# Kernel optimization log

Hardware: AMD Instinct MI355X
Metric: run time of the kernel (lower is better)

## Reference

```python
import jax, jax.numpy as jnp
import numpy as np

EMB = 1024
N_HEAD = 16
D_QK = 128  # emb_dim // h_qk
D_V = 128   # emb_dim // h_v


def setup_inputs() -> dict:
    key = jax.random.key(0)
    ks = jax.random.split(key, 9)
    s_in = 1.0 / np.sqrt(EMB)
    s_pr = 1.0 / np.sqrt(N_HEAD * D_V)
    return {
        "X": jax.random.normal(ks[0], (2, 2048, EMB), dtype=jnp.float32),
        "Wq": jax.random.uniform(ks[1], (EMB, N_HEAD * D_QK), jnp.float32, -s_in, s_in),
        "bq": jax.random.uniform(ks[2], (N_HEAD * D_QK,), jnp.float32, -s_in, s_in),
        "Wk": jax.random.uniform(ks[3], (EMB, N_HEAD * D_QK), jnp.float32, -s_in, s_in),
        "bk": jax.random.uniform(ks[4], (N_HEAD * D_QK,), jnp.float32, -s_in, s_in),
        "Wv": jax.random.uniform(ks[5], (EMB, N_HEAD * D_V), jnp.float32, -s_in, s_in),
        "bv": jax.random.uniform(ks[6], (N_HEAD * D_V,), jnp.float32, -s_in, s_in),
        "Wp": jax.random.uniform(ks[7], (N_HEAD * D_V, EMB), jnp.float32, -s_pr, s_pr),
        "bp": jax.random.uniform(ks[8], (EMB,), jnp.float32, -s_pr, s_pr),
    }


def reference(X, Wq, bq, Wk, bk, Wv, bv, Wp, bp):
    b, t, d = X.shape
    # projections -> (b, h, t, dh)
    Q = (X @ Wq + bq).reshape(b, t, N_HEAD, D_QK).transpose(0, 2, 1, 3)
    K = (X @ Wk + bk).reshape(b, t, N_HEAD, D_QK).transpose(0, 2, 1, 3)
    V = (X @ Wv + bv).reshape(b, t, N_HEAD, D_V).transpose(0, 2, 1, 3)
    scale = 1.0 / jnp.sqrt(jnp.asarray(D_QK, X.dtype))
    att = jnp.einsum("bhqd,bhkd->bhqk", Q, K) * scale  # (b,h,t,t)
    causal = jnp.tril(jnp.ones((t, t), dtype=bool))
    att = jnp.where(causal[None, None], att, jnp.asarray(-jnp.inf, att.dtype))
    att = jax.nn.softmax(att, axis=-1)
    y = jnp.einsum("bhqk,bhkd->bhqd", att, V)
    y = y.transpose(0, 2, 1, 3).reshape(b, t, N_HEAD * D_V)
    return y @ Wp + bp
```

## Files before the change

### kernel.cpp

```cpp
#include <hip/hip_runtime.h>
#include <hip/hip_bf16.h>
#include <math.h>

#define EMB   1024
#define NHEAD 16
#define DHEAD 128
#define TSEQ  2048
#define NB    2
#define MROWS (NB * TSEQ)
#define QKVN  (NHEAD * DHEAD)

typedef __bf16 bf16x8 __attribute__((ext_vector_type(8)));
typedef __bf16 bf16x4 __attribute__((ext_vector_type(4)));
typedef float  f32x4  __attribute__((ext_vector_type(4)));

__global__ __launch_bounds__(256) void cast_to_bf16(
    const float* __restrict__ in, __bf16* __restrict__ out) {
  int i = (blockIdx.x * 256 + threadIdx.x) * 4;
  float4 v = *(const float4*)(in + i);
  bf16x4 o = {(__bf16)v.x, (__bf16)v.y, (__bf16)v.z, (__bf16)v.w};
  *(bf16x4*)(out + i) = o;
}

__global__ __launch_bounds__(256) void cast_transpose(
    const float* __restrict__ in, __bf16* __restrict__ out, int K, int N) {
  __shared__ __bf16 tile[32][33];
  const int k0 = blockIdx.y * 32;
  const int n0 = blockIdx.x * 32;
  const int c = threadIdx.x & 31;
  const int r = threadIdx.x >> 5;
#pragma unroll
  for (int i = 0; i < 4; ++i) {
    int kk = r + i * 8;
    tile[kk][c] = (__bf16)in[(size_t)(k0 + kk) * N + n0 + c];
  }
  __syncthreads();
#pragma unroll
  for (int i = 0; i < 4; ++i) {
    int nn = r + i * 8;
    out[(size_t)(n0 + nn) * K + k0 + c] = tile[c][nn];
  }
}

__global__ __launch_bounds__(256) void transpose_v(
    const __bf16* __restrict__ Vb, __bf16* __restrict__ Vt) {
  __shared__ __bf16 tile[32][34];
  const int bh = blockIdx.z;
  const int b = bh >> 4, h = bh & 15;
  const int t0 = blockIdx.y * 32;
  const int d0 = blockIdx.x * 32;
  const int c = threadIdx.x & 31;
  const int r = threadIdx.x >> 5;
#pragma unroll
  for (int i = 0; i < 4; ++i) {
    int tt = r + i * 8;
    tile[tt][c] = Vb[(size_t)(b * TSEQ + t0 + tt) * QKVN + h * DHEAD + d0 + c];
  }
  __syncthreads();
#pragma unroll
  for (int i = 0; i < 4; ++i) {
    int dd = r + i * 8;
    Vt[((size_t)bh * DHEAD + d0 + dd) * TSEQ + t0 + c] = tile[c][dd];
  }
}

__device__ __forceinline__ void store1(float* p, float v) { *p = v; }
__device__ __forceinline__ void store1(__bf16* p, float v) { *p = (__bf16)v; }

template <typename OT>
__device__ __forceinline__ void gemm_core(
    const __bf16* __restrict__ A, const __bf16* __restrict__ Bt,
    const float* __restrict__ bias, OT* __restrict__ C,
    int N, int K, int brow, int bcol, float osc,
    __bf16* As, __bf16* Bs) {
  const int tid = threadIdx.x;
  const int wv = tid >> 6, ln = tid & 63;
  const int wr = wv >> 1, wc = wv & 1;
  const int cl = ln & 15, gp = ln >> 4;

  f32x4 acc[4][4];
#pragma unroll
  for (int i = 0; i < 4; ++i)
#pragma unroll
    for (int j = 0; j < 4; ++j) acc[i][j] = (f32x4){0.f, 0.f, 0.f, 0.f};

  for (int k0 = 0; k0 < K; k0 += 64) {
#pragma unroll
    for (int i = 0; i < 4; ++i) {
      int idx = i * 256 + tid;
      int r = idx >> 3, cp = idx & 7;
      int c = cp ^ (r & 7);
      const __bf16* ga = A + (size_t)(brow + r) * K + k0 + c * 8;
      __builtin_amdgcn_global_load_lds(
          (const __attribute__((address_space(1))) unsigned int*)ga,
          (__attribute__((address_space(3))) unsigned int*)(As + (size_t)(i * 256 + wv * 64) * 8),
          16, 0, 0);
      const __bf16* gb = Bt + (size_t)(bcol + r) * K + k0 + c * 8;
      __builtin_amdgcn_global_load_lds(
          (const __attribute__((address_space(1))) unsigned int*)gb,
          (__attribute__((address_space(3))) unsigned int*)(Bs + (size_t)(i * 256 + wv * 64) * 8),
          16, 0, 0);
    }
    __syncthreads();

#pragma unroll
    for (int kc = 0; kc < 2; ++kc) {
      bf16x8 af[4], bfr[4];
#pragma unroll
      for (int i = 0; i < 4; ++i) {
        int r = wr * 64 + i * 16 + cl;
        int c = kc * 4 + gp;
        af[i] = *(const bf16x8*)(As + ((size_t)(r * 8 + (c ^ (r & 7)))) * 8);
      }
#pragma unroll
      for (int j = 0; j < 4; ++j) {
        int r = wc * 64 + j * 16 + cl;
        int c = kc * 4 + gp;
        bfr[j] = *(const bf16x8*)(Bs + ((size_t)(r * 8 + (c ^ (r & 7)))) * 8);
      }
#pragma unroll
      for (int i = 0; i < 4; ++i)
#pragma unroll
        for (int j = 0; j < 4; ++j)
          acc[i][j] = __builtin_amdgcn_mfma_f32_16x16x32_bf16(af[i], bfr[j], acc[i][j], 0, 0, 0);
    }
    __syncthreads();
  }

#pragma unroll
  for (int j = 0; j < 4; ++j) {
    int col = bcol + wc * 64 + j * 16 + cl;
    float bb = bias[col];
#pragma unroll
    for (int i = 0; i < 4; ++i) {
#pragma unroll
      for (int rr = 0; rr < 4; ++rr) {
        int row = brow + wr * 64 + i * 16 + gp * 4 + rr;
        store1(C + (size_t)row * N + col, (acc[i][j][rr] + bb) * osc);
      }
    }
  }
}

__global__ __launch_bounds__(256) void gemm_qkv(
    const __bf16* __restrict__ A,
    const __bf16* __restrict__ Wqt, const __bf16* __restrict__ Wkt, const __bf16* __restrict__ Wvt,
    const float* __restrict__ bq, const float* __restrict__ bk, const float* __restrict__ bv,
    __bf16* __restrict__ Q, __bf16* __restrict__ Ko, __bf16* __restrict__ V) {
  __shared__ __bf16 As[8192], Bs[8192];
  const int z = blockIdx.z;
  const __bf16* Bt = z == 0 ? Wqt : z == 1 ? Wkt : Wvt;
  const float* bias = z == 0 ? bq : z == 1 ? bk : bv;
  __bf16* C = z == 0 ? Q : z == 1 ? Ko : V;
  float osc = z == 0 ? 0.08838834764831845f : 1.0f;
  gemm_core<__bf16>(A, Bt, bias, C, QKVN, EMB, blockIdx.y * 128, blockIdx.x * 128, osc, As, Bs);
}

__global__ __launch_bounds__(256) void gemm_proj(
    const __bf16* __restrict__ A, const __bf16* __restrict__ Bt,
    const float* __restrict__ bias, float* __restrict__ C) {
  __shared__ __bf16 As[8192], Bs[8192];
  gemm_core<float>(A, Bt, bias, C, EMB, QKVN, blockIdx.y * 128, blockIdx.x * 128, 1.0f, As, Bs);
}

__device__ __forceinline__ void attn_stage(
    const __bf16* __restrict__ Kg, const __bf16* __restrict__ Vg,
    __bf16* Kbuf, __bf16* Vbuf, int kt, int wv, int ln) {
#pragma unroll
  for (int i = 0; i < 4; ++i) {
    int seg = wv * 4 + i;
    int u = seg * 4 + (ln >> 4);
    int slot = ln & 15;
    int xk = slot ^ (u & 15);
    const __bf16* gk = Kg + (size_t)(kt * 64 + u) * QKVN + xk * 8;
    __builtin_amdgcn_global_load_lds(
        (const __attribute__((address_space(1))) unsigned int*)gk,
        (__attribute__((address_space(3))) unsigned int*)(Kbuf + seg * 512), 16, 0, 0);
    int d = 2 * u + (xk & 1);
    int c2 = xk >> 1;
    const __bf16* gv = Vg + (size_t)d * TSEQ + kt * 64 + c2 * 8;
    __builtin_amdgcn_global_load_lds(
        (const __attribute__((address_space(1))) unsigned int*)gv,
        (__attribute__((address_space(3))) unsigned int*)(Vbuf + seg * 512), 16, 0, 0);
  }
}

__global__ __launch_bounds__(256, 2) void attn_mfma(
    const __bf16* __restrict__ Qb, const __bf16* __restrict__ Kb,
    const __bf16* __restrict__ Vt, __bf16* __restrict__ Y) {
  __shared__ __bf16 Ks[2][8192];
  __shared__ __bf16 Vs[2][8192];
  __shared__ __bf16 Ps[4][2048];

  const int tid = threadIdx.x;
  const int wv = tid >> 6, ln = tid & 63;
  const int cl = ln & 15, gp = ln >> 4;

  const int x = blockIdx.x;
  const int bh = x & 31;
  const int qt = 15 - (x >> 5);
  const int b = bh >> 4, h = bh & 15;
  const int ntiles = 2 * qt + 2;
  const int qloc = qt * 128 + wv * 32;
  const size_t grow = (size_t)b * TSEQ + qloc;

  bf16x8 qa[2][4];
#pragma unroll
  for (int i = 0; i < 2; ++i)
#pragma unroll
    for (int kc = 0; kc < 4; ++kc)
      qa[i][kc] = *(const bf16x8*)(Qb + (grow + i * 16 + cl) * QKVN + h * DHEAD + kc * 32 + gp * 8);

  f32x4 o[2][8];
  f32x4 lacc[2];
#pragma unroll
  for (int i = 0; i < 2; ++i) {
    lacc[i] = (f32x4){0.f, 0.f, 0.f, 0.f};
#pragma unroll
    for (int n = 0; n < 8; ++n) o[i][n] = (f32x4){0.f, 0.f, 0.f, 0.f};
  }
  const __bf16 one_b = (__bf16)1.0f;
  const bf16x8 ones = {one_b, one_b, one_b, one_b, one_b, one_b, one_b, one_b};

  const __bf16* Kg = Kb + (size_t)b * TSEQ * QKVN + h * DHEAD;
  const __bf16* Vg = Vt + (size_t)bh * DHEAD * TSEQ;

  attn_stage(Kg, Vg, Ks[0], Vs[0], 0, wv, ln);
  __syncthreads();

  for (int kt = 0; kt < ntiles; ++kt) {
    const int cur = kt & 1;
    if (kt + 1 < ntiles)
      attn_stage(Kg, Vg, Ks[cur ^ 1], Vs[cur ^ 1], kt + 1, wv, ln);

    if (kt * 64 <= qloc + 31) {
      f32x4 sacc[2][4];
#pragma unroll
      for (int i = 0; i < 2; ++i)
#pragma unroll
        for (int s = 0; s < 4; ++s) sacc[i][s] = (f32x4){0.f, 0.f, 0.f, 0.f};
#pragma unroll
      for (int kc = 0; kc < 4; ++kc) {
#pragma unroll
        for (int s = 0; s < 4; ++s) {
          int r = s * 16 + cl;
          bf16x8 kfr = *(const bf16x8*)(&Ks[cur][r * 128 + (((kc * 4 + gp) ^ (r & 15)) * 8)]);
          sacc[0][s] = __builtin_amdgcn_mfma_f32_16x16x32_bf16(qa[0][kc], kfr, sacc[0][s], 0, 0, 0);
          sacc[1][s] = __builtin_amdgcn_mfma_f32_16x16x32_bf16(qa[1][kc], kfr, sacc[1][s], 0, 0, 0);
        }
      }
      const bool diag = (kt * 64 + 63 > qloc);
#pragma unroll
      for (int i = 0; i < 2; ++i)
#pragma unroll
        for (int s = 0; s < 4; ++s) {
          int key = kt * 64 + s * 16 + cl;
#pragma unroll
          for (int rg = 0; rg < 4; ++rg) {
            int q = i * 16 + gp * 4 + rg;
            float pv = __expf(sacc[i][s][rg]);
            if (diag && key > qloc + q) pv = 0.f;
            Ps[wv][(s * 2 + (cl >> 3)) * 256 + q * 8 + (cl & 7)] = (__bf16)pv;
          }
        }
      bf16x8 pfr[2][2];
#pragma unroll
      for (int i = 0; i < 2; ++i)
#pragma unroll
        for (int k2 = 0; k2 < 2; ++k2)
          pfr[i][k2] = *(const bf16x8*)(&Ps[wv][(k2 * 4 + gp) * 256 + (i * 16 + cl) * 8]);
#pragma unroll
      for (int i = 0; i < 2; ++i)
#pragma unroll
        for (int k2 = 0; k2 < 2; ++k2)
          lacc[i] = __builtin_amdgcn_mfma_f32_16x16x32_bf16(pfr[i][k2], ones, lacc[i], 0, 0, 0);
#pragma unroll
      for (int n = 0; n < 8; ++n) {
#pragma unroll
        for (int k2 = 0; k2 < 2; ++k2) {
          int d = n * 16 + cl;
          int u = d >> 1;
          int xv = ((k2 * 4 + gp) << 1) | (d & 1);
          bf16x8 vfr = *(const bf16x8*)(&Vs[cur][u * 128 + ((xv ^ (u & 15)) * 8)]);
          o[0][n] = __builtin_amdgcn_mfma_f32_16x16x32_bf16(pfr[0][k2], vfr, o[0][n], 0, 0, 0);
          o[1][n] = __builtin_amdgcn_mfma_f32_16x16x32_bf16(pfr[1][k2], vfr, o[1][n], 0, 0, 0);
        }
      }
    }
    __syncthreads();
  }

#pragma unroll
  for (int i = 0; i < 2; ++i) {
    f32x4 inv;
#pragma unroll
    for (int rg = 0; rg < 4; ++rg) inv[rg] = 1.0f / lacc[i][rg];
#pragma unroll
    for (int n = 0; n < 8; ++n)
#pragma unroll
      for (int rg = 0; rg < 4; ++rg) {
        __bf16* yp = Y + (grow + i * 16 + gp * 4 + rg) * QKVN + h * DHEAD + n * 16 + cl;
        *yp = (__bf16)(o[i][n][rg] * inv[rg]);
      }
  }
}

extern "C" void kernel_launch(void* const* d_in, const int* in_sizes, int n_in,
                              void* d_out, int out_size, void* d_ws, size_t ws_size,
                              hipStream_t stream) {
  const float* X  = (const float*)d_in[0];
  const float* Wq = (const float*)d_in[1];
  const float* bq = (const float*)d_in[2];
  const float* Wk = (const float*)d_in[3];
  const float* bk = (const float*)d_in[4];
  const float* Wv = (const float*)d_in[5];
  const float* bv = (const float*)d_in[6];
  const float* Wp = (const float*)d_in[7];
  const float* bp = (const float*)d_in[8];
  float* out = (float*)d_out;

  const size_t xsz = (size_t)MROWS * EMB;
  const size_t wsz = (size_t)EMB * QKVN;
  const size_t msz = (size_t)MROWS * QKVN;
  __bf16* Xb  = (__bf16*)d_ws;
  __bf16* Wqt = Xb + xsz;
  __bf16* Wkt = Wqt + wsz;
  __bf16* Wvt = Wkt + wsz;
  __bf16* Wpt = Wvt + wsz;
  __bf16* Qb  = Wpt + wsz;
  __bf16* Kb  = Qb + msz;
  __bf16* Vb  = Kb + msz;
  __bf16* Vtb = Vb + msz;
  __bf16* Yb  = Vtb + msz;

  dim3 blk(256);

  cast_to_bf16<<<dim3(xsz / 1024), blk, 0, stream>>>(X, Xb);
  cast_transpose<<<dim3(QKVN / 32, EMB / 32), blk, 0, stream>>>(Wq, Wqt, EMB, QKVN);
  cast_transpose<<<dim3(QKVN / 32, EMB / 32), blk, 0, stream>>>(Wk, Wkt, EMB, QKVN);
  cast_transpose<<<dim3(QKVN / 32, EMB / 32), blk, 0, stream>>>(Wv, Wvt, EMB, QKVN);
  cast_transpose<<<dim3(EMB / 32, QKVN / 32), blk, 0, stream>>>(Wp, Wpt, QKVN, EMB);

  gemm_qkv<<<dim3(QKVN / 128, MROWS / 128, 3), blk, 0, stream>>>(
      Xb, Wqt, Wkt, Wvt, bq, bk, bv, Qb, Kb, Vb);

  transpose_v<<<dim3(DHEAD / 32, TSEQ / 32, NB * NHEAD), blk, 0, stream>>>(Vb, Vtb);

  attn_mfma<<<dim3(512), blk, 0, stream>>>(Qb, Kb, Vtb, Yb);

  gemm_proj<<<dim3(EMB / 128, MROWS / 128), blk, 0, stream>>>(Yb, Wpt, bp, out);
}
```

Before: 312.7 us.

## Fuse prep kernels, write V transposed from GEMM, keep P in registers, retile projection

Merges the X cast and the four weight cast-transposes into one prep launch. The QKV GEMM epilogue now writes V directly in head-transposed layout, so the separate transpose_v kernel and its buffer go away. Attention swaps MFMA operand order so P stays in registers: it is built with cross-lane shuffles instead of an LDS round trip, and row sums come from shuffle reductions instead of a ones-matrix MFMA. Output stores are vectorized, and the projection GEMM uses 64-row tiles to double the block count. Several independent changes increase the risk of layout or indexing mistakes.

```diff
diff --git a/kernel.cpp b/kernel.cpp
--- a/kernel.cpp
+++ b/kernel.cpp
@@ -14,60 +14,55 @@
 typedef __bf16 bf16x4 __attribute__((ext_vector_type(4)));
 typedef float  f32x4  __attribute__((ext_vector_type(4)));
 
-__global__ __launch_bounds__(256) void cast_to_bf16(
-    const float* __restrict__ in, __bf16* __restrict__ out) {
-  int i = (blockIdx.x * 256 + threadIdx.x) * 4;
-  float4 v = *(const float4*)(in + i);
-  bf16x4 o = {(__bf16)v.x, (__bf16)v.y, (__bf16)v.z, (__bf16)v.w};
-  *(bf16x4*)(out + i) = o;
-}
-
-__global__ __launch_bounds__(256) void cast_transpose(
-    const float* __restrict__ in, __bf16* __restrict__ out, int K, int N) {
+__device__ __forceinline__ unsigned pk_bf16(float a, float b) {
+  union { __bf16 h; unsigned short u; } ca, cb;
+  ca.h = (__bf16)a; cb.h = (__bf16)b;
+  return (unsigned)ca.u | ((unsigned)cb.u << 16);
+}
+
+__global__ __launch_bounds__(256) void prep(
+    const float* __restrict__ X,
+    const float* __restrict__ Wq, const float* __restrict__ Wk,
+    const float* __restrict__ Wv, const float* __restrict__ Wp,
+    __bf16* __restrict__ Xb, __bf16* __restrict__ Wqt, __bf16* __restrict__ Wkt,
+    __bf16* __restrict__ Wvt, __bf16* __restrict__ Wpt) {
+  const int z = blockIdx.z;
+  if (z == 4) {
+    size_t id = ((size_t)(blockIdx.y * 64 + blockIdx.x)) * 2048 + threadIdx.x * 8;
+    float4 v0 = *(const float4*)(X + id);
+    float4 v1 = *(const float4*)(X + id + 4);
+    bf16x8 o = {(__bf16)v0.x, (__bf16)v0.y, (__bf16)v0.z, (__bf16)v0.w,
+                (__bf16)v1.x, (__bf16)v1.y, (__bf16)v1.z, (__bf16)v1.w};
+    *(bf16x8*)(Xb + id) = o;
+    return;
+  }
   __shared__ __bf16 tile[32][33];
-  const int k0 = blockIdx.y * 32;
-  const int n0 = blockIdx.x * 32;
-  const int c = threadIdx.x & 31;
-  const int r = threadIdx.x >> 5;
+  const float* in; __bf16* out; int K_, N_, k0, n0;
+  if (z < 3) {
+    in = z == 0 ? Wq : z == 1 ? Wk : Wv;
+    out = z == 0 ? Wqt : z == 1 ? Wkt : Wvt;
+    K_ = EMB; N_ = QKVN; k0 = blockIdx.y * 32; n0 = blockIdx.x * 32;
+  } else {
+    in = Wp; out = Wpt; K_ = QKVN; N_ = EMB; k0 = blockIdx.x * 32; n0 = blockIdx.y * 32;
+  }
+  const int c = threadIdx.x & 31, r = threadIdx.x >> 5;
 #pragma unroll
   for (int i = 0; i < 4; ++i) {
     int kk = r + i * 8;
-    tile[kk][c] = (__bf16)in[(size_t)(k0 + kk) * N + n0 + c];
+    tile[kk][c] = (__bf16)in[(size_t)(k0 + kk) * N_ + n0 + c];
   }
   __syncthreads();
 #pragma unroll
   for (int i = 0; i < 4; ++i) {
     int nn = r + i * 8;
-    out[(size_t)(n0 + nn) * K + k0 + c] = tile[c][nn];
-  }
-}
-
-__global__ __launch_bounds__(256) void transpose_v(
-    const __bf16* __restrict__ Vb, __bf16* __restrict__ Vt) {
-  __shared__ __bf16 tile[32][34];
-  const int bh = blockIdx.z;
-  const int b = bh >> 4, h = bh & 15;
-  const int t0 = blockIdx.y * 32;
-  const int d0 = blockIdx.x * 32;
-  const int c = threadIdx.x & 31;
-  const int r = threadIdx.x >> 5;
-#pragma unroll
-  for (int i = 0; i < 4; ++i) {
-    int tt = r + i * 8;
-    tile[tt][c] = Vb[(size_t)(b * TSEQ + t0 + tt) * QKVN + h * DHEAD + d0 + c];
-  }
-  __syncthreads();
-#pragma unroll
-  for (int i = 0; i < 4; ++i) {
-    int dd = r + i * 8;
-    Vt[((size_t)bh * DHEAD + d0 + dd) * TSEQ + t0 + c] = tile[c][dd];
+    out[(size_t)(n0 + nn) * K_ + k0 + c] = tile[c][nn];
   }
 }
 
 __device__ __forceinline__ void store1(float* p, float v) { *p = v; }
 __device__ __forceinline__ void store1(__bf16* p, float v) { *p = (__bf16)v; }
 
-template <typename OT>
+template <int TM, typename OT, bool VT>
 __device__ __forceinline__ void gemm_core(
     const __bf16* __restrict__ A, const __bf16* __restrict__ Bt,
     const float* __restrict__ bias, OT* __restrict__ C,
@@ -75,29 +70,33 @@
     __bf16* As, __bf16* Bs) {
   const int tid = threadIdx.x;
   const int wv = tid >> 6, ln = tid & 63;
-  const int wr = wv >> 1, wc = wv & 1;
   const int cl = ln & 15, gp = ln >> 4;
-
-  f32x4 acc[4][4];
+  constexpr int SJ = (TM == 128) ? 4 : 2;
+  const int rbase = (TM == 128) ? (wv >> 1) * 64 : 0;
+  const int cbase = (TM == 128) ? (wv & 1) * 64 : wv * 32;
+
+  f32x4 acc[4][SJ];
 #pragma unroll
   for (int i = 0; i < 4; ++i)
 #pragma unroll
-    for (int j = 0; j < 4; ++j) acc[i][j] = (f32x4){0.f, 0.f, 0.f, 0.f};
+    for (int j = 0; j < SJ; ++j) acc[i][j] = (f32x4){0.f, 0.f, 0.f, 0.f};
 
   for (int k0 = 0; k0 < K; k0 += 64) {
+#pragma unroll
+    for (int i = 0; i < TM / 32; ++i) {
+      int idx = i * 256 + tid;
+      int r = idx >> 3, cp = idx & 7, c = cp ^ (r & 7);
+      __builtin_amdgcn_global_load_lds(
+          (const __attribute__((address_space(1))) unsigned int*)(A + (size_t)(brow + r) * K + k0 + c * 8),
+          (__attribute__((address_space(3))) unsigned int*)(As + (size_t)(i * 256 + wv * 64) * 8),
+          16, 0, 0);
+    }
 #pragma unroll
     for (int i = 0; i < 4; ++i) {
       int idx = i * 256 + tid;
-      int r = idx >> 3, cp = idx & 7;
-      int c = cp ^ (r & 7);
-      const __bf16* ga = A + (size_t)(brow + r) * K + k0 + c * 8;
+      int r = idx >> 3, cp = idx & 7, c = cp ^ (r & 7);
       __builtin_amdgcn_global_load_lds(
-          (const __attribute__((address_space(1))) unsigned int*)ga,
-          (__attribute__((address_space(3))) unsigned int*)(As + (size_t)(i * 256 + wv * 64) * 8),
-          16, 0, 0);
-      const __bf16* gb = Bt + (size_t)(bcol + r) * K + k0 + c * 8;
-      __builtin_amdgcn_global_load_lds(
-          (const __attribute__((address_space(1))) unsigned int*)gb,
+          (const __attribute__((address_space(1))) unsigned int*)(Bt + (size_t)(bcol + r) * K + k0 + c * 8),
           (__attribute__((address_space(3))) unsigned int*)(Bs + (size_t)(i * 256 + wv * 64) * 8),
           16, 0, 0);
     }
@@ -105,38 +104,56 @@
 
 #pragma unroll
     for (int kc = 0; kc < 2; ++kc) {
-      bf16x8 af[4], bfr[4];
+      bf16x8 af[4], bfr[SJ];
 #pragma unroll
       for (int i = 0; i < 4; ++i) {
-        int r = wr * 64 + i * 16 + cl;
+        int r = rbase + i * 16 + cl;
         int c = kc * 4 + gp;
         af[i] = *(const bf16x8*)(As + ((size_t)(r * 8 + (c ^ (r & 7)))) * 8);
       }
 #pragma unroll
-      for (int j = 0; j < 4; ++j) {
-        int r = wc * 64 + j * 16 + cl;
+      for (int j = 0; j < SJ; ++j) {
+        int r = cbase + j * 16 + cl;
         int c = kc * 4 + gp;
         bfr[j] = *(const bf16x8*)(Bs + ((size_t)(r * 8 + (c ^ (r & 7)))) * 8);
       }
 #pragma unroll
       for (int i = 0; i < 4; ++i)
 #pragma unroll
-        for (int j = 0; j < 4; ++j)
+        for (int j = 0; j < SJ; ++j)
           acc[i][j] = __builtin_amdgcn_mfma_f32_16x16x32_bf16(af[i], bfr[j], acc[i][j], 0, 0, 0);
     }
     __syncthreads();
   }
 
-#pragma unroll
-  for (int j = 0; j < 4; ++j) {
-    int col = bcol + wc * 64 + j * 16 + cl;
-    float bb = bias[col];
-#pragma unroll
-    for (int i = 0; i < 4; ++i) {
-#pragma unroll
-      for (int rr = 0; rr < 4; ++rr) {
-        int row = brow + wr * 64 + i * 16 + gp * 4 + rr;
-        store1(C + (size_t)row * N + col, (acc[i][j][rr] + bb) * osc);
+  if constexpr (VT) {
+#pragma unroll
+    for (int j = 0; j < SJ; ++j) {
+      int col = bcol + cbase + j * 16 + cl;
+      float bb = bias[col];
+      int hh = col >> 7, dh = col & 127;
+#pragma unroll
+      for (int i = 0; i < 4; ++i) {
+        int row = brow + rbase + i * 16 + gp * 4;
+        int bi = row >> 11, t = row & 2047;
+        __bf16* p = (__bf16*)C + ((size_t)((bi * NHEAD + hh) * DHEAD + dh)) * TSEQ + t;
+        bf16x4 st = {(__bf16)((acc[i][j][0] + bb) * osc), (__bf16)((acc[i][j][1] + bb) * osc),
+                     (__bf16)((acc[i][j][2] + bb) * osc), (__bf16)((acc[i][j][3] + bb) * osc)};
+        *(bf16x4*)p = st;
+      }
+    }
+  } else {
+#pragma unroll
+    for (int j = 0; j < SJ; ++j) {
+      int col = bcol + cbase + j * 16 + cl;
+      float bb = bias[col];
+#pragma unroll
+      for (int i = 0; i < 4; ++i) {
+#pragma unroll
+        for (int rr = 0; rr < 4; ++rr) {
+          int row = brow + rbase + i * 16 + gp * 4 + rr;
+          store1(C + (size_t)row * N + col, (acc[i][j][rr] + bb) * osc);
+        }
       }
     }
   }
@@ -146,21 +163,27 @@
     const __bf16* __restrict__ A,
     const __bf16* __restrict__ Wqt, const __bf16* __restrict__ Wkt, const __bf16* __restrict__ Wvt,
     const float* __restrict__ bq, const float* __restrict__ bk, const float* __restrict__ bv,
-    __bf16* __restrict__ Q, __bf16* __restrict__ Ko, __bf16* __restrict__ V) {
+    __bf16* __restrict__ Q, __bf16* __restrict__ Ko, __bf16* __restrict__ Vt) {
   __shared__ __bf16 As[8192], Bs[8192];
   const int z = blockIdx.z;
-  const __bf16* Bt = z == 0 ? Wqt : z == 1 ? Wkt : Wvt;
-  const float* bias = z == 0 ? bq : z == 1 ? bk : bv;
-  __bf16* C = z == 0 ? Q : z == 1 ? Ko : V;
-  float osc = z == 0 ? 0.08838834764831845f : 1.0f;
-  gemm_core<__bf16>(A, Bt, bias, C, QKVN, EMB, blockIdx.y * 128, blockIdx.x * 128, osc, As, Bs);
+  if (z == 0) {
+    gemm_core<128, __bf16, false>(A, Wqt, bq, Q, QKVN, EMB, blockIdx.y * 128, blockIdx.x * 128,
+                                  0.08838834764831845f, As, Bs);
+  } else if (z == 1) {
+    gemm_core<128, __bf16, false>(A, Wkt, bk, Ko, QKVN, EMB, blockIdx.y * 128, blockIdx.x * 128,
+                                  1.0f, As, Bs);
+  } else {
+    gemm_core<128, __bf16, true>(A, Wvt, bv, Vt, QKVN, EMB, blockIdx.y * 128, blockIdx.x * 128,
+                                 1.0f, As, Bs);
+  }
 }
 
 __global__ __launch_bounds__(256) void gemm_proj(
     const __bf16* __restrict__ A, const __bf16* __restrict__ Bt,
     const float* __restrict__ bias, float* __restrict__ C) {
-  __shared__ __bf16 As[8192], Bs[8192];
-  gemm_core<float>(A, Bt, bias, C, EMB, QKVN, blockIdx.y * 128, blockIdx.x * 128, 1.0f, As, Bs);
+  __shared__ __bf16 As[4096], Bs[8192];
+  gemm_core<64, float, false>(A, Bt, bias, C, EMB, QKVN, blockIdx.y * 64, blockIdx.x * 128,
+                              1.0f, As, Bs);
 }
 
 __device__ __forceinline__ void attn_stage(
@@ -172,15 +195,12 @@
     int u = seg * 4 + (ln >> 4);
     int slot = ln & 15;
     int xk = slot ^ (u & 15);
-    const __bf16* gk = Kg + (size_t)(kt * 64 + u) * QKVN + xk * 8;
     __builtin_amdgcn_global_load_lds(
-        (const __attribute__((address_space(1))) unsigned int*)gk,
+        (const __attribute__((address_space(1))) unsigned int*)(Kg + (size_t)(kt * 64 + u) * QKVN + xk * 8),
         (__attribute__((address_space(3))) unsigned int*)(Kbuf + seg * 512), 16, 0, 0);
-    int d = 2 * u + (xk & 1);
-    int c2 = xk >> 1;
-    const __bf16* gv = Vg + (size_t)d * TSEQ + kt * 64 + c2 * 8;
+    int d = 2 * u + (xk & 1), c2 = xk >> 1;
     __builtin_amdgcn_global_load_lds(
-        (const __attribute__((address_space(1))) unsigned int*)gv,
+        (const __attribute__((address_space(1))) unsigned int*)(Vg + (size_t)d * TSEQ + kt * 64 + c2 * 8),
         (__attribute__((address_space(3))) unsigned int*)(Vbuf + seg * 512), 16, 0, 0);
   }
 }
@@ -190,7 +210,6 @@
     const __bf16* __restrict__ Vt, __bf16* __restrict__ Y) {
   __shared__ __bf16 Ks[2][8192];
   __shared__ __bf16 Vs[2][8192];
-  __shared__ __bf16 Ps[4][2048];
 
   const int tid = threadIdx.x;
   const int wv = tid >> 6, ln = tid & 63;
@@ -212,21 +231,21 @@
       qa[i][kc] = *(const bf16x8*)(Qb + (grow + i * 16 + cl) * QKVN + h * DHEAD + kc * 32 + gp * 8);
 
   f32x4 o[2][8];
-  f32x4 lacc[2];
-#pragma unroll
-  for (int i = 0; i < 2; ++i) {
-    lacc[i] = (f32x4){0.f, 0.f, 0.f, 0.f};
+#pragma unroll
+  for (int i = 0; i < 2; ++i)
 #pragma unroll
     for (int n = 0; n < 8; ++n) o[i][n] = (f32x4){0.f, 0.f, 0.f, 0.f};
-  }
-  const __bf16 one_b = (__bf16)1.0f;
-  const bf16x8 ones = {one_b, one_b, one_b, one_b, one_b, one_b, one_b, one_b};
+  float l[2] = {0.f, 0.f};
 
   const __bf16* Kg = Kb + (size_t)b * TSEQ * QKVN + h * DHEAD;
   const __bf16* Vg = Vt + (size_t)bh * DHEAD * TSEQ;
 
   attn_stage(Kg, Vg, Ks[0], Vs[0], 0, wv, ln);
   __syncthreads();
+
+  const int m0 = 32 * (gp & 1) + cl;
+  const int m1 = m0 + 16;
+  const bool hi = gp >= 2;
 
   for (int kt = 0; kt < ntiles; ++kt) {
     const int cur = kt & 1;
@@ -245,45 +264,58 @@
         for (int s = 0; s < 4; ++s) {
           int r = s * 16 + cl;
           bf16x8 kfr = *(const bf16x8*)(&Ks[cur][r * 128 + (((kc * 4 + gp) ^ (r & 15)) * 8)]);
-          sacc[0][s] = __builtin_amdgcn_mfma_f32_16x16x32_bf16(qa[0][kc], kfr, sacc[0][s], 0, 0, 0);
-          sacc[1][s] = __builtin_amdgcn_mfma_f32_16x16x32_bf16(qa[1][kc], kfr, sacc[1][s], 0, 0, 0);
+          sacc[0][s] = __builtin_amdgcn_mfma_f32_16x16x32_bf16(kfr, qa[0][kc], sacc[0][s], 0, 0, 0);
+          sacc[1][s] = __builtin_amdgcn_mfma_f32_16x16x32_bf16(kfr, qa[1][kc], sacc[1][s], 0, 0, 0);
         }
       }
       const bool diag = (kt * 64 + 63 > qloc);
-#pragma unroll
-      for (int i = 0; i < 2; ++i)
+      unsigned pk[2][4][2];
+#pragma unroll
+      for (int i = 0; i < 2; ++i) {
+        float psum = 0.f;
+        int q = qloc + i * 16 + cl;
 #pragma unroll
         for (int s = 0; s < 4; ++s) {
-          int key = kt * 64 + s * 16 + cl;
+          float e[4];
 #pragma unroll
           for (int rg = 0; rg < 4; ++rg) {
-            int q = i * 16 + gp * 4 + rg;
-            float pv = __expf(sacc[i][s][rg]);
-            if (diag && key > qloc + q) pv = 0.f;
-            Ps[wv][(s * 2 + (cl >> 3)) * 256 + q * 8 + (cl & 7)] = (__bf16)pv;
+            e[rg] = __expf(sacc[i][s][rg]);
+            if (diag && (kt * 64 + s * 16 + gp * 4 + rg) > q) e[rg] = 0.f;
+            psum += e[rg];
           }
-        }
-      bf16x8 pfr[2][2];
-#pragma unroll
-      for (int i = 0; i < 2; ++i)
-#pragma unroll
-        for (int k2 = 0; k2 < 2; ++k2)
-          pfr[i][k2] = *(const bf16x8*)(&Ps[wv][(k2 * 4 + gp) * 256 + (i * 16 + cl) * 8]);
-#pragma unroll
-      for (int i = 0; i < 2; ++i)
-#pragma unroll
-        for (int k2 = 0; k2 < 2; ++k2)
-          lacc[i] = __builtin_amdgcn_mfma_f32_16x16x32_bf16(pfr[i][k2], ones, lacc[i], 0, 0, 0);
-#pragma unroll
-      for (int n = 0; n < 8; ++n) {
-#pragma unroll
-        for (int k2 = 0; k2 < 2; ++k2) {
-          int d = n * 16 + cl;
+          pk[i][s][0] = pk_bf16(e[0], e[1]);
+          pk[i][s][1] = pk_bf16(e[2], e[3]);
+        }
+        psum += __shfl_xor(psum, 16, 64);
+        psum += __shfl_xor(psum, 32, 64);
+        l[i] += psum;
+      }
+#pragma unroll
+      for (int k2 = 0; k2 < 2; ++k2) {
+        union PU { unsigned u[4]; bf16x8 v; } pf[2];
+#pragma unroll
+        for (int i = 0; i < 2; ++i) {
+          unsigned a0 = __shfl(pk[i][2 * k2][0], m0, 64);
+          unsigned b0 = __shfl(pk[i][2 * k2 + 1][0], m0, 64);
+          unsigned a1 = __shfl(pk[i][2 * k2][1], m0, 64);
+          unsigned b1 = __shfl(pk[i][2 * k2 + 1][1], m0, 64);
+          unsigned a2 = __shfl(pk[i][2 * k2][0], m1, 64);
+          unsigned b2 = __shfl(pk[i][2 * k2 + 1][0], m1, 64);
+          unsigned a3 = __shfl(pk[i][2 * k2][1], m1, 64);
+          unsigned b3 = __shfl(pk[i][2 * k2 + 1][1], m1, 64);
+          pf[i].u[0] = hi ? b0 : a0;
+          pf[i].u[1] = hi ? b1 : a1;
+          pf[i].u[2] = hi ? b2 : a2;
+          pf[i].u[3] = hi ? b3 : a3;
+        }
+#pragma unroll
+        for (int ds = 0; ds < 8; ++ds) {
+          int d = ds * 16 + cl;
           int u = d >> 1;
           int xv = ((k2 * 4 + gp) << 1) | (d & 1);
           bf16x8 vfr = *(const bf16x8*)(&Vs[cur][u * 128 + ((xv ^ (u & 15)) * 8)]);
-          o[0][n] = __builtin_amdgcn_mfma_f32_16x16x32_bf16(pfr[0][k2], vfr, o[0][n], 0, 0, 0);
-          o[1][n] = __builtin_amdgcn_mfma_f32_16x16x32_bf16(pfr[1][k2], vfr, o[1][n], 0, 0, 0);
+          o[0][ds] = __builtin_amdgcn_mfma_f32_16x16x32_bf16(vfr, pf[0].v, o[0][ds], 0, 0, 0);
+          o[1][ds] = __builtin_amdgcn_mfma_f32_16x16x32_bf16(vfr, pf[1].v, o[1][ds], 0, 0, 0);
         }
       }
     }
@@ -292,16 +324,14 @@
 
 #pragma unroll
   for (int i = 0; i < 2; ++i) {
-    f32x4 inv;
-#pragma unroll
-    for (int rg = 0; rg < 4; ++rg) inv[rg] = 1.0f / lacc[i][rg];
-#pragma unroll
-    for (int n = 0; n < 8; ++n)
-#pragma unroll
-      for (int rg = 0; rg < 4; ++rg) {
-        __bf16* yp = Y + (grow + i * 16 + gp * 4 + rg) * QKVN + h * DHEAD + n * 16 + cl;
-        *yp = (__bf16)(o[i][n][rg] * inv[rg]);
-      }
+    float inv = 1.0f / l[i];
+    __bf16* yrow = Y + (grow + i * 16 + cl) * QKVN + h * DHEAD;
+#pragma unroll
+    for (int ds = 0; ds < 8; ++ds) {
+      bf16x4 st = {(__bf16)(o[i][ds][0] * inv), (__bf16)(o[i][ds][1] * inv),
+                   (__bf16)(o[i][ds][2] * inv), (__bf16)(o[i][ds][3] * inv)};
+      *(bf16x4*)(yrow + ds * 16 + gp * 4) = st;
+    }
   }
 }
 
@@ -329,24 +359,17 @@
   __bf16* Wpt = Wvt + wsz;
   __bf16* Qb  = Wpt + wsz;
   __bf16* Kb  = Qb + msz;
-  __bf16* Vb  = Kb + msz;
-  __bf16* Vtb = Vb + msz;
+  __bf16* Vtb = Kb + msz;
   __bf16* Yb  = Vtb + msz;
 
   dim3 blk(256);
 
-  cast_to_bf16<<<dim3(xsz / 1024), blk, 0, stream>>>(X, Xb);
-  cast_transpose<<<dim3(QKVN / 32, EMB / 32), blk, 0, stream>>>(Wq, Wqt, EMB, QKVN);
-  cast_transpose<<<dim3(QKVN / 32, EMB / 32), blk, 0, stream>>>(Wk, Wkt, EMB, QKVN);
-  cast_transpose<<<dim3(QKVN / 32, EMB / 32), blk, 0, stream>>>(Wv, Wvt, EMB, QKVN);
-  cast_transpose<<<dim3(EMB / 32, QKVN / 32), blk, 0, stream>>>(Wp, Wpt, QKVN, EMB);
+  prep<<<dim3(64, 32, 5), blk, 0, stream>>>(X, Wq, Wk, Wv, Wp, Xb, Wqt, Wkt, Wvt, Wpt);
 
   gemm_qkv<<<dim3(QKVN / 128, MROWS / 128, 3), blk, 0, stream>>>(
-      Xb, Wqt, Wkt, Wvt, bq, bk, bv, Qb, Kb, Vb);
-
-  transpose_v<<<dim3(DHEAD / 32, TSEQ / 32, NB * NHEAD), blk, 0, stream>>>(Vb, Vtb);
+      Xb, Wqt, Wkt, Wvt, bq, bk, bv, Qb, Kb, Vtb);
 
   attn_mfma<<<dim3(512), blk, 0, stream>>>(Qb, Kb, Vtb, Yb);
 
-  gemm_proj<<<dim3(EMB / 128, MROWS / 128), blk, 0, stream>>>(Yb, Wpt, bp, out);
-}
+  gemm_proj<<<dim3(EMB / 128, MROWS / 64), blk, 0, stream>>>(Yb, Wpt, bp, out);
+}
```

Measured after the change: 284.9 us. 8.9% less time.
